# Kernel optimization log

Measured on AMD Instinct MI355X. Metric: run time of the kernel, lower is better.

Reference implementation:

```python
import jax, jax.numpy as jnp
import numpy as np

B, S, D = 2, 2048, 2048
H, G = 32, 8          # num_heads, num_kv_groups
GS = H // G           # group_size = 4
HD = D // H           # head_dim = 64


def setup_inputs() -> dict:
    key = jax.random.key(0)
    ks = jax.random.split(key, 5)
    x = jax.random.normal(ks[0], (B, S, D), dtype=jnp.float32)
    Wq = jax.random.normal(ks[1], (D, D), dtype=jnp.float32) * 0.02
    Wk = jax.random.normal(ks[2], (G * HD, D), dtype=jnp.float32) * 0.02
    Wv = jax.random.normal(ks[3], (G * HD, D), dtype=jnp.float32) * 0.02
    Wo = jax.random.normal(ks[4], (D, D), dtype=jnp.float32) * 0.02
    return {"x": x, "Wq": Wq, "Wk": Wk, "Wv": Wv, "Wo": Wo}


def reference(x, Wq, Wk, Wv, Wo):
    b, s, _ = x.shape
    # Projections (nn.Linear: x @ W.T, no bias)
    # queries: view(b,s,H,HD) with head h = g*GS + j -> reshape to (b,s,G,GS,HD)
    q = (x @ Wq.T).reshape(b, s, G, GS, HD)
    k = (x @ Wk.T).reshape(b, s, G, HD)   # [b, s, G, HD]
    v = (x @ Wv.T).reshape(b, s, G, HD)
    # repeat_interleave(group_size, dim=heads): head h uses kv group h // GS,
    # which is exactly the grouped einsum below (no materialized repeat).
    scores = jnp.einsum('bqgjd,bkgd->bgjqk', q, k) / np.sqrt(HD).astype(np.float32)
    # prefill cache: ptr=0, so mask is plain causal (q_pos < k_pos masked out)
    qpos = jnp.arange(s)
    mask = qpos[:, None] < qpos[None, :]        # [s, s], True = masked
    scores = jnp.where(mask, -jnp.inf, scores)
    w = jax.nn.softmax(scores, axis=-1)         # dropout p=0.0 (eval)
    ctx = jnp.einsum('bgjqk,bkgd->bqgjd', w, v).reshape(b, s, D)
    return ctx @ Wo.T
```

## Files before the change

### kernel.cpp

```cpp
#include <hip/hip_runtime.h>
#include <hip/hip_bf16.h>

typedef unsigned short u16;
typedef short bf16x4 __attribute__((ext_vector_type(4)));
typedef short bf16x8 __attribute__((ext_vector_type(8)));
typedef float f32x4 __attribute__((ext_vector_type(4)));

#define NEG_BIG (-1e30f)
#define SCL 0.18033688f

__device__ __forceinline__ u16 f2bf(float f) {
    union { float f; unsigned int u; } x; x.f = f;
    unsigned int r = x.u + 0x7fffu + ((x.u >> 16) & 1u);
    return (u16)(r >> 16);
}

__device__ __forceinline__ unsigned cvtpk(float lo, float hi) {
    unsigned r;
    asm("v_cvt_pk_bf16_f32 %0, %1, %2" : "=v"(r) : "v"(lo), "v"(hi));
    return r;
}

__device__ __forceinline__ f32x4 mfma16(bf16x4 a, bf16x4 b, f32x4 c) {
#if __has_builtin(__builtin_amdgcn_mfma_f32_16x16x16bf16_1k)
    return __builtin_amdgcn_mfma_f32_16x16x16bf16_1k(a, b, c, 0, 0, 0);
#else
    asm("v_mfma_f32_16x16x16_bf16 %0, %1, %2, %0" : "+v"(c) : "v"(a), "v"(b));
    return c;
#endif
}

__device__ __forceinline__ void dma16(const u16* g, const u16* lds) {
    __builtin_amdgcn_global_load_lds(
        (const __attribute__((address_space(1))) unsigned int*)g,
        (__attribute__((address_space(3))) unsigned int*)lds, 16, 0, 0);
}

__device__ __forceinline__ bf16x8 sfrag(const u16* lds, int row, int kb8) {
    int slot = row * 8 + (kb8 ^ (row & 7));
    return *(const bf16x8*)(lds + slot * 8);
}

__device__ __forceinline__ bf16x4 vfrag(const u16* lds, int row, int kb, int lhi) {
    int c = kb * 2 + (lhi >> 1);
    int slot = row * 8 + (c ^ (row & 7));
    return *(const bf16x4*)(lds + slot * 8 + (lhi & 1) * 4);
}

__global__ __launch_bounds__(256) void cvt_all(const float* __restrict__ x,
                                               const float* __restrict__ wq,
                                               const float* __restrict__ wk,
                                               const float* __restrict__ wv,
                                               const float* __restrict__ wo,
                                               u16* __restrict__ xb, u16* __restrict__ wqb,
                                               u16* __restrict__ wkb, u16* __restrict__ wvb,
                                               u16* __restrict__ wob) {
    size_t i = (size_t)blockIdx.x * 256 + threadIdx.x;
    const float* s; u16* d; size_t off;
    if      (i < 1048576) { s = x;  d = xb;  off = i; }
    else if (i < 1572864) { s = wq; d = wqb; off = i - 1048576; }
    else if (i < 1703936) { s = wk; d = wkb; off = i - 1572864; }
    else if (i < 1835008) { s = wv; d = wvb; off = i - 1703936; }
    else                  { s = wo; d = wob; off = i - 1835008; }
    const float* p = s + off * 8;
    float4 a = *(const float4*)p;
    float4 b = *(const float4*)(p + 4);
    union { unsigned u[4]; bf16x8 v; } r;
    r.u[0] = cvtpk(a.x, a.y);
    r.u[1] = cvtpk(a.z, a.w);
    r.u[2] = cvtpk(b.x, b.y);
    r.u[3] = cvtpk(b.z, b.w);
    *(bf16x8*)(d + off * 8) = r.v;
}

__global__ __launch_bounds__(256) void gemm_bt(const u16* __restrict__ A,
                                               const u16* __restrict__ Bt,
                                               float* __restrict__ C,
                                               int M, int N, int K) {
    __shared__ u16 As[8192];
    __shared__ u16 Bs[8192];
    const int t = threadIdx.x;
    const int wave = t >> 6, lane = t & 63;
    const int wm = (wave >> 1) * 64, wn = (wave & 1) * 64;
    const int lhi = lane >> 4, llo = lane & 15;
    const int m0 = blockIdx.y * 128, n0 = blockIdx.x * 128;
    const int wbase = wave * 64;

    f32x4 acc[4][4] = {};
    for (int k0 = 0; k0 < K; k0 += 64) {
        const u16* Ab = A + (size_t)m0 * K + k0;
        const u16* Bb = Bt + (size_t)n0 * K + k0;
#pragma unroll
        for (int i = 0; i < 4; ++i) {
            int s = i * 256 + t;
            int row = s >> 3, gch = (s & 7) ^ (row & 7);
            dma16(Ab + (size_t)row * K + gch * 8, As + (i * 256 + wbase) * 8);
            dma16(Bb + (size_t)row * K + gch * 8, Bs + (i * 256 + wbase) * 8);
        }
        __syncthreads();
#pragma unroll
        for (int ks = 0; ks < 2; ++ks) {
            const int kb = ks * 4 + lhi;
            bf16x8 af[4], bfg[4];
#pragma unroll
            for (int mi = 0; mi < 4; ++mi) af[mi] = sfrag(As, wm + mi * 16 + llo, kb);
#pragma unroll
            for (int ni = 0; ni < 4; ++ni) bfg[ni] = sfrag(Bs, wn + ni * 16 + llo, kb);
#pragma unroll
            for (int mi = 0; mi < 4; ++mi)
#pragma unroll
                for (int ni = 0; ni < 4; ++ni)
                    acc[mi][ni] = __builtin_amdgcn_mfma_f32_16x16x32_bf16(
                        af[mi], bfg[ni], acc[mi][ni], 0, 0, 0);
        }
        __syncthreads();
    }
#pragma unroll
    for (int mi = 0; mi < 4; ++mi)
#pragma unroll
        for (int ni = 0; ni < 4; ++ni)
#pragma unroll
            for (int r = 0; r < 4; ++r) {
                int row = m0 + wm + mi * 16 + lhi * 4 + r;
                int col = n0 + wn + ni * 16 + llo;
                C[(size_t)row * N + col] = acc[mi][ni][r];
            }
}

__global__ __launch_bounds__(256) void gemm_qkv(const u16* __restrict__ A,
                                                const u16* __restrict__ Wq,
                                                const u16* __restrict__ Wk,
                                                const u16* __restrict__ Wv,
                                                u16* __restrict__ Qout,
                                                u16* __restrict__ Kout,
                                                u16* __restrict__ Vtout) {
    const int K = 2048;
    __shared__ u16 As[8192];
    __shared__ u16 Bs[8192];
    const int t = threadIdx.x;
    const int wave = t >> 6, lane = t & 63;
    const int wm = (wave >> 1) * 64, wn = (wave & 1) * 64;
    const int lhi = lane >> 4, llo = lane & 15;
    const int m0 = blockIdx.y * 128;
    const int bx = blockIdx.x;
    const int kind = (bx < 16) ? 0 : (bx < 20 ? 1 : 2);
    const int n0 = (kind == 0) ? bx * 128 : (bx & 3) * 128;
    const u16* Bt = ((kind == 0) ? Wq : (kind == 1) ? Wk : Wv) + (size_t)n0 * K;
    const int wbase = wave * 64;

    f32x4 acc[4][4] = {};
    for (int k0 = 0; k0 < K; k0 += 64) {
        const u16* Ab = A + (size_t)m0 * K + k0;
        const u16* Bb = Bt + k0;
#pragma unroll
        for (int i = 0; i < 4; ++i) {
            int s = i * 256 + t;
            int row = s >> 3, gch = (s & 7) ^ (row & 7);
            dma16(Ab + (size_t)row * K + gch * 8, As + (i * 256 + wbase) * 8);
            dma16(Bb + (size_t)row * K + gch * 8, Bs + (i * 256 + wbase) * 8);
        }
        __syncthreads();
#pragma unroll
        for (int ks = 0; ks < 2; ++ks) {
            const int kb = ks * 4 + lhi;
            bf16x8 af[4], bfg[4];
#pragma unroll
            for (int mi = 0; mi < 4; ++mi) af[mi] = sfrag(As, wm + mi * 16 + llo, kb);
#pragma unroll
            for (int ni = 0; ni < 4; ++ni) bfg[ni] = sfrag(Bs, wn + ni * 16 + llo, kb);
#pragma unroll
            for (int mi = 0; mi < 4; ++mi)
#pragma unroll
                for (int ni = 0; ni < 4; ++ni)
                    acc[mi][ni] = __builtin_amdgcn_mfma_f32_16x16x32_bf16(
                        af[mi], bfg[ni], acc[mi][ni], 0, 0, 0);
        }
        __syncthreads();
    }

    if (kind == 0) {
#pragma unroll
        for (int mi = 0; mi < 4; ++mi)
#pragma unroll
            for (int ni = 0; ni < 4; ++ni)
#pragma unroll
                for (int r = 0; r < 4; ++r) {
                    int row = m0 + wm + mi * 16 + lhi * 4 + r;
                    int col = n0 + wn + ni * 16 + llo;
                    Qout[(size_t)row * 2048 + col] = f2bf(acc[mi][ni][r] * SCL);
                }
    } else if (kind == 1) {
#pragma unroll
        for (int mi = 0; mi < 4; ++mi)
#pragma unroll
            for (int ni = 0; ni < 4; ++ni)
#pragma unroll
                for (int r = 0; r < 4; ++r) {
                    int row = m0 + wm + mi * 16 + lhi * 4 + r;
                    int col = n0 + wn + ni * 16 + llo;
                    Kout[(size_t)row * 512 + col] = f2bf(acc[mi][ni][r]);
                }
    } else {
#pragma unroll
        for (int mi = 0; mi < 4; ++mi)
#pragma unroll
            for (int ni = 0; ni < 4; ++ni) {
                int row = m0 + wm + mi * 16 + lhi * 4;
                int col = n0 + wn + ni * 16 + llo;
                size_t off = ((size_t)col + (size_t)(row >> 11) * 512) * 2048 + (row & 2047);
                union { unsigned u[2]; short4 s; } v;
                v.u[0] = cvtpk(acc[mi][ni][0], acc[mi][ni][1]);
                v.u[1] = cvtpk(acc[mi][ni][2], acc[mi][ni][3]);
                *(short4*)(Vtout + off) = v.s;
            }
    }
}

__global__ __launch_bounds__(256, 4) void attn6(const u16* __restrict__ Q,
                                                const u16* __restrict__ Kbuf,
                                                const u16* __restrict__ Vtb,
                                                u16* __restrict__ Ctx) {
    __shared__ u16 Ks[2][4096];
    __shared__ u16 Vs[2][4096];
    const int bg = blockIdx.y;
    const int b = bg >> 3, g = bg & 7;
    const int t = threadIdx.x, w = t >> 6, lane = t & 63;
    const int lhi = lane >> 4, llo = lane & 15;
    const int h = g * 4 + w;
    const int wbase = w * 64;

    const u16* Kp = Kbuf + (size_t)(b * 2048) * 512 + g * 64;
    const u16* Vp = Vtb + (size_t)bg * 64 * 2048;

    const int r0 = t >> 3,          g0 = (t & 7) ^ (r0 & 7);
    const int r1 = (256 + t) >> 3,  g1 = ((256 + t) & 7) ^ (r1 & 7);

    bf16x4 ones;
    ones[0] = ones[1] = ones[2] = ones[3] = (short)0x3F80;

    auto STAGE = [&](int kt, int bufi) {
        const u16* Kt = Kp + (size_t)kt * 64 * 512;
        const u16* Vt2 = Vp + kt * 64;
        u16* Kd = Ks[bufi]; u16* Vd = Vs[bufi];
        dma16(Kt + (size_t)r0 * 512 + g0 * 8, Kd + wbase * 8);
        dma16(Vt2 + (size_t)r0 * 2048 + g0 * 8, Vd + wbase * 8);
        dma16(Kt + (size_t)r1 * 512 + g1 * 8, Kd + (256 + wbase) * 8);
        dma16(Vt2 + (size_t)r1 * 2048 + g1 * 8, Vd + (256 + wbase) * 8);
    };

#pragma unroll
    for (int ph = 0; ph < 2; ++ph) {
        const int qt = ph ? (int)blockIdx.x : 127 - (int)blockIdx.x;

        const u16* Qp = Q + ((size_t)(b * 2048 + qt * 16)) * 2048 + h * 64;
        bf16x8 aq[2];
#pragma unroll
        for (int ks = 0; ks < 2; ++ks)
            aq[ks] = *(const bf16x8*)(Qp + (size_t)llo * 2048 + ks * 32 + lhi * 8);

        f32x4 o[4] = {};
        f32x4 lac = {};
        float m_ = NEG_BIG;

        const int ktmax = (qt * 16 + 15) >> 6;

        STAGE(0, 0);
        asm volatile("s_waitcnt vmcnt(0)" ::: "memory");
        __builtin_amdgcn_s_barrier();

        for (int kt = 0; kt <= ktmax; ++kt) {
            const int cur = kt & 1;
            if (kt < ktmax) STAGE(kt + 1, cur ^ 1);
            const u16* Ksb = Ks[cur];
            const u16* Vsb = Vs[cur];

            f32x4 st[4] = {};
            __builtin_amdgcn_s_setprio(1);
#pragma unroll
            for (int ks = 0; ks < 2; ++ks) {
                const int kb8 = ks * 4 + lhi;
                bf16x8 kf[4];
#pragma unroll
                for (int kb = 0; kb < 4; ++kb) kf[kb] = sfrag(Ksb, kb * 16 + llo, kb8);
#pragma unroll
                for (int kb = 0; kb < 4; ++kb)
                    st[kb] = __builtin_amdgcn_mfma_f32_16x16x32_bf16(
                        kf[kb], aq[ks], st[kb], 0, 0, 0);
            }
            __builtin_amdgcn_s_setprio(0);

            if (kt * 64 + 63 > qt * 16) {
                int qg = qt * 16 + llo;
#pragma unroll
                for (int kb = 0; kb < 4; ++kb)
#pragma unroll
                    for (int r = 0; r < 4; ++r) {
                        int kg = kt * 64 + kb * 16 + lhi * 4 + r;
                        if (kg > qg) st[kb][r] = NEG_BIG;
                    }
            }

            float t0 = fmaxf(fmaxf(st[0][0], st[0][1]), st[0][2]);
            float t1 = fmaxf(fmaxf(st[0][3], st[1][0]), st[1][1]);
            float t2 = fmaxf(fmaxf(st[1][2], st[1][3]), st[2][0]);
            float t3 = fmaxf(fmaxf(st[2][1], st[2][2]), st[2][3]);
            float t4 = fmaxf(fmaxf(st[3][0], st[3][1]), st[3][2]);
            float mx = fmaxf(fmaxf(fmaxf(t0, t1), t2),
                             fmaxf(fmaxf(t3, t4), st[3][3]));
            mx = fmaxf(mx, __shfl_xor(mx, 16, 64));
            mx = fmaxf(mx, __shfl_xor(mx, 32, 64));

            if (__any(mx > m_ + 8.0f)) {
                float mn = fmaxf(m_, mx);
                float alpha = exp2f(m_ - mn);
                m_ = mn;
#pragma unroll
                for (int hb = 0; hb < 4; ++hb) o[hb] *= alpha;
                lac *= alpha;
            }

            bf16x4 pf[4];
#pragma unroll
            for (int kb = 0; kb < 4; ++kb) {
                float p0 = exp2f(st[kb][0] - m_);
                float p1 = exp2f(st[kb][1] - m_);
                float p2 = exp2f(st[kb][2] - m_);
                float p3 = exp2f(st[kb][3] - m_);
                union { unsigned u[2]; bf16x4 v; } pu;
                pu.u[0] = cvtpk(p0, p1);
                pu.u[1] = cvtpk(p2, p3);
                pf[kb] = pu.v;
            }

            __builtin_amdgcn_s_setprio(1);
#pragma unroll
            for (int kb = 0; kb < 4; ++kb) lac = mfma16(ones, pf[kb], lac);
#pragma unroll
            for (int kb = 0; kb < 4; ++kb)
#pragma unroll
                for (int hb = 0; hb < 4; ++hb)
                    o[hb] = mfma16(vfrag(Vsb, hb * 16 + llo, kb, lhi), pf[kb], o[hb]);
            __builtin_amdgcn_s_setprio(0);

            asm volatile("s_waitcnt vmcnt(0)" ::: "memory");
            __builtin_amdgcn_s_barrier();
        }

        float inv = 1.0f / lac[0];
        u16* Cp = Ctx + (size_t)(b * 2048 + qt * 16) * 2048 + h * 64;
#pragma unroll
        for (int hb = 0; hb < 4; ++hb) {
            union { unsigned u[2]; short4 s; } cu;
            cu.u[0] = cvtpk(o[hb][0] * inv, o[hb][1] * inv);
            cu.u[1] = cvtpk(o[hb][2] * inv, o[hb][3] * inv);
            *(short4*)(Cp + (size_t)llo * 2048 + hb * 16 + lhi * 4) = cu.s;
        }
    }
}

extern "C" void kernel_launch(void* const* d_in, const int* in_sizes, int n_in,
                              void* d_out, int out_size, void* d_ws, size_t ws_size,
                              hipStream_t stream) {
    const float* x  = (const float*)d_in[0];
    const float* Wq = (const float*)d_in[1];
    const float* Wk = (const float*)d_in[2];
    const float* Wv = (const float*)d_in[3];
    const float* Wo = (const float*)d_in[4];

    u16* xb  = (u16*)d_ws;
    u16* wqb = xb + 8388608;
    u16* wkb = wqb + 4194304;
    u16* wvb = wkb + 1048576;
    u16* wob = wvb + 1048576;
    u16* Kb  = wob + 4194304;
    u16* Vtb = Kb + 2097152;
    u16* Ctx = xb;
    u16* Qb  = (u16*)d_out;
    float* out = (float*)d_out;

    cvt_all<<<dim3(9216), 256, 0, stream>>>(x, Wq, Wk, Wv, Wo, xb, wqb, wkb, wvb, wob);
    gemm_qkv<<<dim3(24, 32), 256, 0, stream>>>(xb, wqb, wkb, wvb, Qb, Kb, Vtb);
    attn6<<<dim3(64, 16), 256, 0, stream>>>(Qb, Kb, Vtb, Ctx);
    gemm_bt<<<dim3(16, 32), 256, 0, stream>>>(Ctx, wob, out, 4096, 2048, 2048);
}
```

Measured before the change: 312.9 us.

## Process paired query tiles concurrently sharing K/V staging and remap block order

Before, each block handled two query tiles one after the other and loaded K/V separately for each. Now the long tile (127-x) and the short tile (x) are processed in the same key loop, so every K/V tile loaded into LDS and every V fragment serves both, while the short tile still does work only up to its own causal limit. The grid becomes 1D with a remap that places the four blocks of consecutive x for one batch/group next to each other, likely to improve L2 reuse of K/V. The cost is higher register pressure from two sets of accumulators and softmax state, which could reduce occupancy or cause spills.

```diff
diff --git a/kernel.cpp b/kernel.cpp
--- a/kernel.cpp
+++ b/kernel.cpp
@@ -216,13 +216,15 @@
     }
 }
 
-__global__ __launch_bounds__(256, 4) void attn6(const u16* __restrict__ Q,
+__global__ __launch_bounds__(256, 4) void attn7(const u16* __restrict__ Q,
                                                 const u16* __restrict__ Kbuf,
                                                 const u16* __restrict__ Vtb,
                                                 u16* __restrict__ Ctx) {
     __shared__ u16 Ks[2][4096];
     __shared__ u16 Vs[2][4096];
-    const int bg = blockIdx.y;
+    const int bid = (int)blockIdx.x;
+    const int x  = ((bid >> 6) << 2) | (bid & 3);
+    const int bg = (bid >> 2) & 15;
     const int b = bg >> 3, g = bg & 7;
     const int t = threadIdx.x, w = t >> 6, lane = t & 63;
     const int lhi = lane >> 4, llo = lane & 15;
@@ -248,32 +250,36 @@
         dma16(Vt2 + (size_t)r1 * 2048 + g1 * 8, Vd + (256 + wbase) * 8);
     };
 
-#pragma unroll
-    for (int ph = 0; ph < 2; ++ph) {
-        const int qt = ph ? (int)blockIdx.x : 127 - (int)blockIdx.x;
-
-        const u16* Qp = Q + ((size_t)(b * 2048 + qt * 16)) * 2048 + h * 64;
-        bf16x8 aq[2];
-#pragma unroll
-        for (int ks = 0; ks < 2; ++ks)
-            aq[ks] = *(const bf16x8*)(Qp + (size_t)llo * 2048 + ks * 32 + lhi * 8);
-
-        f32x4 o[4] = {};
-        f32x4 lac = {};
-        float m_ = NEG_BIG;
-
-        const int ktmax = (qt * 16 + 15) >> 6;
-
-        STAGE(0, 0);
-        asm volatile("s_waitcnt vmcnt(0)" ::: "memory");
-        __builtin_amdgcn_s_barrier();
-
-        for (int kt = 0; kt <= ktmax; ++kt) {
-            const int cur = kt & 1;
-            if (kt < ktmax) STAGE(kt + 1, cur ^ 1);
-            const u16* Ksb = Ks[cur];
-            const u16* Vsb = Vs[cur];
-
+    const int qa = 127 - x, qb = x;
+    const int ktmax_a = (qa * 16 + 15) >> 6;
+    const int ktmax_b = (qb * 16 + 15) >> 6;
+
+    const u16* Qpa = Q + ((size_t)(b * 2048 + qa * 16)) * 2048 + h * 64;
+    const u16* Qpb = Q + ((size_t)(b * 2048 + qb * 16)) * 2048 + h * 64;
+    bf16x8 aqa[2], aqb[2];
+#pragma unroll
+    for (int ks = 0; ks < 2; ++ks) {
+        aqa[ks] = *(const bf16x8*)(Qpa + (size_t)llo * 2048 + ks * 32 + lhi * 8);
+        aqb[ks] = *(const bf16x8*)(Qpb + (size_t)llo * 2048 + ks * 32 + lhi * 8);
+    }
+
+    f32x4 oa[4] = {}, ob[4] = {};
+    f32x4 laca = {}, lacb = {};
+    float ma = NEG_BIG, mb = NEG_BIG;
+
+    STAGE(0, 0);
+    asm volatile("s_waitcnt vmcnt(0)" ::: "memory");
+    __builtin_amdgcn_s_barrier();
+
+    for (int kt = 0; kt <= ktmax_a; ++kt) {
+        const int cur = kt & 1;
+        if (kt < ktmax_a) STAGE(kt + 1, cur ^ 1);
+        const u16* Ksb = Ks[cur];
+        const u16* Vsb = Vs[cur];
+        const bool doB = (kt <= ktmax_b);
+
+        bf16x4 pfa[4], pfb[4];
+        {
             f32x4 st[4] = {};
             __builtin_amdgcn_s_setprio(1);
 #pragma unroll
@@ -285,12 +291,11 @@
 #pragma unroll
                 for (int kb = 0; kb < 4; ++kb)
                     st[kb] = __builtin_amdgcn_mfma_f32_16x16x32_bf16(
-                        kf[kb], aq[ks], st[kb], 0, 0, 0);
+                        kf[kb], aqa[ks], st[kb], 0, 0, 0);
             }
             __builtin_amdgcn_s_setprio(0);
-
-            if (kt * 64 + 63 > qt * 16) {
-                int qg = qt * 16 + llo;
+            if (kt * 64 + 63 > qa * 16) {
+                int qg = qa * 16 + llo;
 #pragma unroll
                 for (int kb = 0; kb < 4; ++kb)
 #pragma unroll
@@ -299,7 +304,6 @@
                         if (kg > qg) st[kb][r] = NEG_BIG;
                     }
             }
-
             float t0 = fmaxf(fmaxf(st[0][0], st[0][1]), st[0][2]);
             float t1 = fmaxf(fmaxf(st[0][3], st[1][0]), st[1][1]);
             float t2 = fmaxf(fmaxf(st[1][2], st[1][3]), st[2][0]);
@@ -309,50 +313,133 @@
                              fmaxf(fmaxf(t3, t4), st[3][3]));
             mx = fmaxf(mx, __shfl_xor(mx, 16, 64));
             mx = fmaxf(mx, __shfl_xor(mx, 32, 64));
-
-            if (__any(mx > m_ + 8.0f)) {
-                float mn = fmaxf(m_, mx);
-                float alpha = exp2f(m_ - mn);
-                m_ = mn;
-#pragma unroll
-                for (int hb = 0; hb < 4; ++hb) o[hb] *= alpha;
-                lac *= alpha;
-            }
-
-            bf16x4 pf[4];
+            if (__any(mx > ma + 8.0f)) {
+                float mn = fmaxf(ma, mx);
+                float alpha = exp2f(ma - mn);
+                ma = mn;
+#pragma unroll
+                for (int hb = 0; hb < 4; ++hb) oa[hb] *= alpha;
+                laca *= alpha;
+            }
 #pragma unroll
             for (int kb = 0; kb < 4; ++kb) {
-                float p0 = exp2f(st[kb][0] - m_);
-                float p1 = exp2f(st[kb][1] - m_);
-                float p2 = exp2f(st[kb][2] - m_);
-                float p3 = exp2f(st[kb][3] - m_);
+                float p0 = exp2f(st[kb][0] - ma);
+                float p1 = exp2f(st[kb][1] - ma);
+                float p2 = exp2f(st[kb][2] - ma);
+                float p3 = exp2f(st[kb][3] - ma);
                 union { unsigned u[2]; bf16x4 v; } pu;
                 pu.u[0] = cvtpk(p0, p1);
                 pu.u[1] = cvtpk(p2, p3);
-                pf[kb] = pu.v;
-            }
-
+                pfa[kb] = pu.v;
+            }
+        }
+
+        if (doB) {
+            f32x4 st[4] = {};
             __builtin_amdgcn_s_setprio(1);
 #pragma unroll
-            for (int kb = 0; kb < 4; ++kb) lac = mfma16(ones, pf[kb], lac);
+            for (int ks = 0; ks < 2; ++ks) {
+                const int kb8 = ks * 4 + lhi;
+                bf16x8 kf[4];
+#pragma unroll
+                for (int kb = 0; kb < 4; ++kb) kf[kb] = sfrag(Ksb, kb * 16 + llo, kb8);
+#pragma unroll
+                for (int kb = 0; kb < 4; ++kb)
+                    st[kb] = __builtin_amdgcn_mfma_f32_16x16x32_bf16(
+                        kf[kb], aqb[ks], st[kb], 0, 0, 0);
+            }
+            __builtin_amdgcn_s_setprio(0);
+            if (kt * 64 + 63 > qb * 16) {
+                int qg = qb * 16 + llo;
+#pragma unroll
+                for (int kb = 0; kb < 4; ++kb)
+#pragma unroll
+                    for (int r = 0; r < 4; ++r) {
+                        int kg = kt * 64 + kb * 16 + lhi * 4 + r;
+                        if (kg > qg) st[kb][r] = NEG_BIG;
+                    }
+            }
+            float t0 = fmaxf(fmaxf(st[0][0], st[0][1]), st[0][2]);
+            float t1 = fmaxf(fmaxf(st[0][3], st[1][0]), st[1][1]);
+            float t2 = fmaxf(fmaxf(st[1][2], st[1][3]), st[2][0]);
+            float t3 = fmaxf(fmaxf(st[2][1], st[2][2]), st[2][3]);
+            float t4 = fmaxf(fmaxf(st[3][0], st[3][1]), st[3][2]);
+            float mx = fmaxf(fmaxf(fmaxf(t0, t1), t2),
+                             fmaxf(fmaxf(t3, t4), st[3][3]));
+            mx = fmaxf(mx, __shfl_xor(mx, 16, 64));
+            mx = fmaxf(mx, __shfl_xor(mx, 32, 64));
+            if (__any(mx > mb + 8.0f)) {
+                float mn = fmaxf(mb, mx);
+                float alpha = exp2f(mb - mn);
+                mb = mn;
+#pragma unroll
+                for (int hb = 0; hb < 4; ++hb) ob[hb] *= alpha;
+                lacb *= alpha;
+            }
+#pragma unroll
+            for (int kb = 0; kb < 4; ++kb) {
+                float p0 = exp2f(st[kb][0] - mb);
+                float p1 = exp2f(st[kb][1] - mb);
+                float p2 = exp2f(st[kb][2] - mb);
+                float p3 = exp2f(st[kb][3] - mb);
+                union { unsigned u[2]; bf16x4 v; } pu;
+                pu.u[0] = cvtpk(p0, p1);
+                pu.u[1] = cvtpk(p2, p3);
+                pfb[kb] = pu.v;
+            }
+        }
+
+        __builtin_amdgcn_s_setprio(1);
+        if (doB) {
+#pragma unroll
+            for (int kb = 0; kb < 4; ++kb) {
+                laca = mfma16(ones, pfa[kb], laca);
+                lacb = mfma16(ones, pfb[kb], lacb);
+            }
 #pragma unroll
             for (int kb = 0; kb < 4; ++kb)
 #pragma unroll
-                for (int hb = 0; hb < 4; ++hb)
-                    o[hb] = mfma16(vfrag(Vsb, hb * 16 + llo, kb, lhi), pf[kb], o[hb]);
-            __builtin_amdgcn_s_setprio(0);
-
-            asm volatile("s_waitcnt vmcnt(0)" ::: "memory");
-            __builtin_amdgcn_s_barrier();
-        }
-
-        float inv = 1.0f / lac[0];
-        u16* Cp = Ctx + (size_t)(b * 2048 + qt * 16) * 2048 + h * 64;
+                for (int hb = 0; hb < 4; ++hb) {
+                    bf16x4 vf = vfrag(Vsb, hb * 16 + llo, kb, lhi);
+                    oa[hb] = mfma16(vf, pfa[kb], oa[hb]);
+                    ob[hb] = mfma16(vf, pfb[kb], ob[hb]);
+                }
+        } else {
+#pragma unroll
+            for (int kb = 0; kb < 4; ++kb) laca = mfma16(ones, pfa[kb], laca);
+#pragma unroll
+            for (int kb = 0; kb < 4; ++kb)
+#pragma unroll
+                for (int hb = 0; hb < 4; ++hb) {
+                    bf16x4 vf = vfrag(Vsb, hb * 16 + llo, kb, lhi);
+                    oa[hb] = mfma16(vf, pfa[kb], oa[hb]);
+                }
+        }
+        __builtin_amdgcn_s_setprio(0);
+
+        asm volatile("s_waitcnt vmcnt(0)" ::: "memory");
+        __builtin_amdgcn_s_barrier();
+    }
+
+    {
+        float inv = 1.0f / laca[0];
+        u16* Cp = Ctx + (size_t)(b * 2048 + qa * 16) * 2048 + h * 64;
 #pragma unroll
         for (int hb = 0; hb < 4; ++hb) {
             union { unsigned u[2]; short4 s; } cu;
-            cu.u[0] = cvtpk(o[hb][0] * inv, o[hb][1] * inv);
-            cu.u[1] = cvtpk(o[hb][2] * inv, o[hb][3] * inv);
+            cu.u[0] = cvtpk(oa[hb][0] * inv, oa[hb][1] * inv);
+            cu.u[1] = cvtpk(oa[hb][2] * inv, oa[hb][3] * inv);
+            *(short4*)(Cp + (size_t)llo * 2048 + hb * 16 + lhi * 4) = cu.s;
+        }
+    }
+    {
+        float inv = 1.0f / lacb[0];
+        u16* Cp = Ctx + (size_t)(b * 2048 + qb * 16) * 2048 + h * 64;
+#pragma unroll
+        for (int hb = 0; hb < 4; ++hb) {
+            union { unsigned u[2]; short4 s; } cu;
+            cu.u[0] = cvtpk(ob[hb][0] * inv, ob[hb][1] * inv);
+            cu.u[1] = cvtpk(ob[hb][2] * inv, ob[hb][3] * inv);
             *(short4*)(Cp + (size_t)llo * 2048 + hb * 16 + lhi * 4) = cu.s;
         }
     }
@@ -380,6 +467,6 @@
 
     cvt_all<<<dim3(9216), 256, 0, stream>>>(x, Wq, Wk, Wv, Wo, xb, wqb, wkb, wvb, wob);
     gemm_qkv<<<dim3(24, 32), 256, 0, stream>>>(xb, wqb, wkb, wvb, Qb, Kb, Vtb);
-    attn6<<<dim3(64, 16), 256, 0, stream>>>(Qb, Kb, Vtb, Ctx);
+    attn7<<<dim3(1024), 256, 0, stream>>>(Qb, Kb, Vtb, Ctx);
     gemm_bt<<<dim3(16, 32), 256, 0, stream>>>(Ctx, wob, out, 4096, 2048, 2048);
 }
```

New measurement: 364.4 us. 1.16x slower.
